# Optimization experiments

Measured on AMD Instinct MI355X. Metric: run time of the kernel, lower is better.

Reference implementation:

```python
import jax, jax.numpy as jnp
import numpy as np

N_NODES = 100000
N_EDGES = 600000
D = 128


def setup_inputs() -> dict:
    key = jax.random.key(0)
    k1, k2, k3, k4, k5, k6 = jax.random.split(key, 6)
    feat = jax.random.normal(k1, (N_NODES, D), dtype=jnp.float32)
    src = jax.random.randint(k2, (N_EDGES,), 0, N_NODES, dtype=jnp.int64)
    dst = jax.random.randint(k3, (N_EDGES,), 0, N_NODES, dtype=jnp.int64)
    W_neigh = jax.random.normal(k4, (D, D), dtype=jnp.float32) * (1.0 / np.sqrt(D))
    b_neigh = jax.random.normal(k5, (D,), dtype=jnp.float32) * 0.02
    W_self = jax.random.normal(k6, (D, D), dtype=jnp.float32) * (1.0 / np.sqrt(D))
    return {"feat": feat, "src": src, "dst": dst,
            "W_neigh": W_neigh, "b_neigh": b_neigh, "W_self": W_self}


def reference(feat, src, dst, W_neigh, b_neigh, W_self):
    # DGL GraphConv(norm='none'): sum-aggregate neighbor features, then linear.
    # agg[i] = sum_{(s->i) in E} feat[s]
    agg = jax.ops.segment_sum(feat[src], dst, num_segments=feat.shape[0])  # [N, D]
    neigh_feat = agg @ W_neigh + b_neigh                                   # [N, Dout]
    self_feat = feat @ W_self                                              # [N, Dout]
    return neigh_feat + self_feat
```

## Files before the change

kernel.cpp:

```cpp
#include <hip/hip_runtime.h>

#define DF 128
#define CAP 16
#define GR 64

typedef __attribute__((ext_vector_type(8))) short short8;
typedef __attribute__((ext_vector_type(4))) float v4f;

__device__ __forceinline__ unsigned short f2bf(float x) {
    unsigned u = __float_as_uint(x);
    unsigned r = (u + 0x7FFFu + ((u >> 16) & 1u)) >> 16;
    return (unsigned short)r;
}
__device__ __forceinline__ float bf2f(unsigned short h) {
    return __uint_as_float((unsigned)h << 16);
}
__device__ __forceinline__ unsigned pack2(float a, float b) {
    return (unsigned)f2bf(a) | ((unsigned)f2bf(b) << 16);
}

__global__ __launch_bounds__(256) void prep_kernel(
    const int* __restrict__ idx32, int nE, int* __restrict__ hdr,
    const float* __restrict__ Wn, const float* __restrict__ Ws,
    unsigned short* __restrict__ Bt, int* __restrict__ counts, int cnt_ints)
{
    const int b = blockIdx.x;
    const int t = threadIdx.x;
    if (b == 0) {
        __shared__ int sh;
        if (t == 0) sh = 0;
        __syncthreads();
        int found = 0;
        for (int i = t; i < 2048 && i < nE; i += 256)
            if (idx32[2 * i + 1] != 0) found = 1;
        if (found) sh = 1;
        __syncthreads();
        if (t == 0) { hdr[0] = sh; hdr[1] = 0; }
    } else if (b <= 128) {
        int idx = (b - 1) * 256 + t;
        int n = idx >> 7, k = idx & 127;
        float v = (n < DF) ? Wn[(size_t)k * DF + n] : Ws[(size_t)k * DF + (n - DF)];
        Bt[idx] = f2bf(v);
    } else {
        int off = ((b - 129) * 256 + t) * 4;
        if (off < cnt_ints)
            *reinterpret_cast<int4*>(counts + off) = make_int4(0, 0, 0, 0);
    }
}

__global__ __launch_bounds__(256) void fused_kernel(
    const float* __restrict__ feat, const unsigned short* __restrict__ Bt,
    const float* __restrict__ bias, unsigned short* __restrict__ Ybf,
    float* __restrict__ out, int M,
    const void* __restrict__ src, const void* __restrict__ dst, int nE,
    int* __restrict__ hdr, int* __restrict__ counts, int* __restrict__ buckets,
    int2* __restrict__ ovf)
{
    const int t   = threadIdx.x;
    const int bid = blockIdx.x;
    const int nb  = (int)gridDim.x;

    {
        const int e0 = (int)((long long)bid * nE / nb);
        const int e1 = (int)((long long)(bid + 1) * nE / nb);
        const int is32 = hdr[0];
        if (is32) {
            const int* sp = (const int*)src;
            const int* dp = (const int*)dst;
            for (int e = e0 + t; e < e1; e += 256) {
                int s = sp[e], d = dp[e];
                int pos = atomicAdd(&counts[d], 1);
                if (pos < CAP) {
                    buckets[(size_t)d * CAP + pos] = s;
                } else {
                    int oi = atomicAdd(&hdr[1], 1);
                    ovf[oi] = make_int2(s, d);
                }
            }
        } else {
            const long long* sp = (const long long*)src;
            const long long* dp = (const long long*)dst;
            for (int e = e0 + t; e < e1; e += 256) {
                int s = (int)sp[e], d = (int)dp[e];
                int pos = atomicAdd(&counts[d], 1);
                if (pos < CAP) {
                    buckets[(size_t)d * CAP + pos] = s;
                } else {
                    int oi = atomicAdd(&hdr[1], 1);
                    ovf[oi] = make_int2(s, d);
                }
            }
        }
    }

    __shared__ unsigned short As[GR][136];
    __shared__ unsigned short Ys[GR][136];

    const int wave = t >> 6;
    const int lane = t & 63;
    const int nl   = lane & 15;
    const int quad = lane >> 4;
    const int block_row = bid * GR;

    {
        const float* base = feat + (size_t)block_row * DF;
#pragma unroll
        for (int it = 0; it < 8; it++) {
            const int idx = t * 4 + it * 1024;
            const int row = idx >> 7, col = idx & 127;
            float4 v;
            if (block_row + row < M)
                v = *reinterpret_cast<const float4*>(base + idx);
            else
                v = make_float4(0.f, 0.f, 0.f, 0.f);
            uint2 pk;
            pk.x = pack2(v.x, v.y);
            pk.y = pack2(v.z, v.w);
            *reinterpret_cast<uint2*>(&As[row][col]) = pk;
        }
    }

    const int n0 = wave * 64;
    short8 bfrag[4][4];
#pragma unroll
    for (int ct = 0; ct < 4; ct++)
#pragma unroll
        for (int kk = 0; kk < 4; kk++)
            bfrag[ct][kk] = *reinterpret_cast<const short8*>(
                Bt + (size_t)(n0 + ct * 16 + nl) * DF + kk * 32 + quad * 8);

    float bcol[4];
#pragma unroll
    for (int ct = 0; ct < 4; ct++) {
        int n = n0 + ct * 16 + nl;
        bcol[ct] = (n >= DF) ? bias[n - DF] : 0.f;
    }

    __syncthreads();

#pragma unroll
    for (int rt = 0; rt < 4; rt++) {
        short8 afrag[4];
#pragma unroll
        for (int kk = 0; kk < 4; kk++)
            afrag[kk] = *reinterpret_cast<const short8*>(
                &As[rt * 16 + nl][kk * 32 + quad * 8]);
#pragma unroll
        for (int ct = 0; ct < 4; ct++) {
            v4f acc = {0.f, 0.f, 0.f, 0.f};
#pragma unroll
            for (int kk = 0; kk < 4; kk++)
                acc = __builtin_amdgcn_mfma_f32_16x16x32_bf16(
                    afrag[kk], bfrag[ct][kk], acc, 0, 0, 0);
            const int n = n0 + ct * 16 + nl;
            const int lrow = rt * 16 + quad * 4;
            if (n < DF) {
#pragma unroll
                for (int r = 0; r < 4; r++)
                    Ys[lrow + r][n] = f2bf(acc[r]);
            } else {
#pragma unroll
                for (int r = 0; r < 4; r++) {
                    const int grow = block_row + lrow + r;
                    if (grow < M)
                        out[(size_t)grow * DF + (n - DF)] = acc[r] + bcol[ct];
                }
            }
        }
    }

    __syncthreads();

    {
        const int row = t >> 2;
        const int cb  = (t & 3) * 32;
        const int grow = block_row + row;
        if (grow < M) {
            const uint4* srcp = reinterpret_cast<const uint4*>(&Ys[row][cb]);
            uint4* dstp = reinterpret_cast<uint4*>(Ybf + (size_t)grow * DF + cb);
            dstp[0] = srcp[0];
            dstp[1] = srcp[1];
            dstp[2] = srcp[2];
            dstp[3] = srcp[3];
        }
    }
}

__global__ __launch_bounds__(256) void gather_kernel(
    const unsigned short* __restrict__ Ybf,
    const int* __restrict__ counts, const int* __restrict__ buckets,
    const int* __restrict__ hdr, const int2* __restrict__ ovf,
    float* __restrict__ out, int M, int ngroups)
{
    const int gid  = blockIdx.x * 256 + threadIdx.x;
    const int grp  = gid >> 4;
    const int lane = gid & 15;
    const size_t lo = (size_t)lane * 8;

#define LDY(s) (*reinterpret_cast<const uint4*>(Ybf + (size_t)(s) * DF + lo))
#define ACC8(Y) do { \
        a0 += bf2f((unsigned short)((Y).x)); a1 += bf2f((unsigned short)((Y).x >> 16)); \
        a2 += bf2f((unsigned short)((Y).y)); a3 += bf2f((unsigned short)((Y).y >> 16)); \
        a4 += bf2f((unsigned short)((Y).z)); a5 += bf2f((unsigned short)((Y).z >> 16)); \
        a6 += bf2f((unsigned short)((Y).w)); a7 += bf2f((unsigned short)((Y).w >> 16)); \
    } while (0)

    if (grp < M) {
        const int node = grp;
        const int deg_raw = counts[node];
        const int deg = min(deg_raw, CAP);
        const int* b = buckets + (size_t)node * CAP;

        float a0 = 0.f, a1 = 0.f, a2 = 0.f, a3 = 0.f;
        float a4 = 0.f, a5 = 0.f, a6 = 0.f, a7 = 0.f;

        int4 sa = *reinterpret_cast<const int4*>(b);
        int4 sb = *reinterpret_cast<const int4*>(b + 4);
        uint4 y0, y1, y2, y3, y4, y5, y6, y7;
        if (0 < deg) y0 = LDY(sa.x);
        if (1 < deg) y1 = LDY(sa.y);
        if (2 < deg) y2 = LDY(sa.z);
        if (3 < deg) y3 = LDY(sa.w);
        if (4 < deg) y4 = LDY(sb.x);
        if (5 < deg) y5 = LDY(sb.y);
        if (6 < deg) y6 = LDY(sb.z);
        if (7 < deg) y7 = LDY(sb.w);
        if (0 < deg) ACC8(y0);
        if (1 < deg) ACC8(y1);
        if (2 < deg) ACC8(y2);
        if (3 < deg) ACC8(y3);
        if (4 < deg) ACC8(y4);
        if (5 < deg) ACC8(y5);
        if (6 < deg) ACC8(y6);
        if (7 < deg) ACC8(y7);

        if (deg > 8) {
            int4 sc = *reinterpret_cast<const int4*>(b + 8);
            int4 sd = *reinterpret_cast<const int4*>(b + 12);
            uint4 z0, z1, z2, z3, z4, z5, z6, z7;
            if ( 8 < deg) z0 = LDY(sc.x);
            if ( 9 < deg) z1 = LDY(sc.y);
            if (10 < deg) z2 = LDY(sc.z);
            if (11 < deg) z3 = LDY(sc.w);
            if (12 < deg) z4 = LDY(sd.x);
            if (13 < deg) z5 = LDY(sd.y);
            if (14 < deg) z6 = LDY(sd.z);
            if (15 < deg) z7 = LDY(sd.w);
            if ( 8 < deg) ACC8(z0);
            if ( 9 < deg) ACC8(z1);
            if (10 < deg) ACC8(z2);
            if (11 < deg) ACC8(z3);
            if (12 < deg) ACC8(z4);
            if (13 < deg) ACC8(z5);
            if (14 < deg) ACC8(z6);
            if (15 < deg) ACC8(z7);
        }

        float* op = out + (size_t)node * DF + lo;
        if (deg_raw <= CAP) {
            float4 o0 = *reinterpret_cast<const float4*>(op);
            float4 o1 = *reinterpret_cast<const float4*>(op + 4);
            o0.x += a0; o0.y += a1; o0.z += a2; o0.w += a3;
            o1.x += a4; o1.y += a5; o1.z += a6; o1.w += a7;
            *reinterpret_cast<float4*>(op)     = o0;
            *reinterpret_cast<float4*>(op + 4) = o1;
        } else {
            unsafeAtomicAdd(op + 0, a0);
            unsafeAtomicAdd(op + 1, a1);
            unsafeAtomicAdd(op + 2, a2);
            unsafeAtomicAdd(op + 3, a3);
            unsafeAtomicAdd(op + 4, a4);
            unsafeAtomicAdd(op + 5, a5);
            unsafeAtomicAdd(op + 6, a6);
            unsafeAtomicAdd(op + 7, a7);
        }
    }

    int n_ovf = hdr[1];
    for (int i = grp; i < n_ovf; i += ngroups) {
        int2 sd = ovf[i];
        uint4 y = LDY(sd.x);
        float* p = out + (size_t)sd.y * DF + lo;
        unsafeAtomicAdd(p + 0, bf2f((unsigned short)(y.x)));
        unsafeAtomicAdd(p + 1, bf2f((unsigned short)(y.x >> 16)));
        unsafeAtomicAdd(p + 2, bf2f((unsigned short)(y.y)));
        unsafeAtomicAdd(p + 3, bf2f((unsigned short)(y.y >> 16)));
        unsafeAtomicAdd(p + 4, bf2f((unsigned short)(y.z)));
        unsafeAtomicAdd(p + 5, bf2f((unsigned short)(y.z >> 16)));
        unsafeAtomicAdd(p + 6, bf2f((unsigned short)(y.w)));
        unsafeAtomicAdd(p + 7, bf2f((unsigned short)(y.w >> 16)));
    }
#undef LDY
#undef ACC8
}

extern "C" void kernel_launch(void* const* d_in, const int* in_sizes, int n_in,
                              void* d_out, int out_size, void* d_ws, size_t ws_size,
                              hipStream_t stream) {
    const float* feat = (const float*)d_in[0];
    const void*  src  = d_in[1];
    const void*  dst  = d_in[2];
    const float* Wn   = (const float*)d_in[3];
    const float* bias = (const float*)d_in[4];
    const float* Wsf  = (const float*)d_in[5];
    float* out = (float*)d_out;

    const int M  = in_sizes[0] / DF;
    const int nE = in_sizes[1];

    const size_t cnt_off   = 256;
    const size_t cnt_bytes = (((size_t)(M + 1) * 4) + 255) & ~(size_t)255;
    const size_t bkt_off   = cnt_off + cnt_bytes;
    const size_t bkt_bytes = (size_t)M * CAP * sizeof(int);
    const size_t bt_off    = (bkt_off + bkt_bytes + 255) & ~(size_t)255;
    const size_t bt_bytes  = (size_t)256 * DF * sizeof(unsigned short);
    const size_t y_off     = bt_off + bt_bytes;
    const size_t y_bytes   = (size_t)M * DF * sizeof(unsigned short);
    const size_t ovf_off   = (y_off + y_bytes + 255) & ~(size_t)255;

    int*            hdr     = (int*)d_ws;
    int*            counts  = (int*)((char*)d_ws + cnt_off);
    int*            buckets = (int*)((char*)d_ws + bkt_off);
    unsigned short* Bt      = (unsigned short*)((char*)d_ws + bt_off);
    unsigned short* Ybf     = (unsigned short*)((char*)d_ws + y_off);
    int2*           ovf     = (int2*)((char*)d_ws + ovf_off);

    const int cnt_ints = (int)(cnt_bytes / 4);
    const int nzb = (cnt_ints + 1023) / 1024;
    prep_kernel<<<1 + 128 + nzb, 256, 0, stream>>>(
        (const int*)src, nE, hdr, Wn, Wsf, Bt, counts, cnt_ints);

    const int gemm_blocks = (M + GR - 1) / GR;
    fused_kernel<<<gemm_blocks, 256, 0, stream>>>(
        feat, Bt, bias, Ybf, out, M, src, dst, nE,
        hdr, counts, buckets, ovf);

    const int gablocks = (int)(((long long)M * 16 + 255) / 256);
    const int ngroups  = gablocks * 16;
    gather_kernel<<<gablocks, 256, 0, stream>>>(
        Ybf, counts, buckets, hdr, ovf, out, M, ngroups);
}
```

Before: 204.5 us.

## Merge scatter, GEMM and gather into a persistent cooperative kernel

Replaces the fused scatter+GEMM launch and the separate gather launch with one persistent cooperative kernel. Blocks pull work items (edge-placement slices and GEMM tiles) from an atomic counter, then meet at a grid-wide sync before a grid-stride gather. The gather now loads the out rows early and adds scheduling barriers to group its loads ahead of the accumulation. This saves a kernel launch and its tail, at the cost of grid-sync overhead and occupancy limits (launch_bounds 256,4). A fallback two-kernel path runs if the cooperative launch fails.

Result: slower. 348.3 us (+70.3%).

```diff
diff --git a/kernel.cpp b/kernel.cpp
--- a/kernel.cpp
+++ b/kernel.cpp
@@ -1,8 +1,12 @@
 #include <hip/hip_runtime.h>
+#include <hip/hip_cooperative_groups.h>
+
+namespace cg = cooperative_groups;
 
 #define DF 128
 #define CAP 16
 #define GR 64
+#define PSLICES 256
 
 typedef __attribute__((ext_vector_type(8))) short short8;
 typedef __attribute__((ext_vector_type(4))) float v4f;
@@ -35,7 +39,7 @@
             if (idx32[2 * i + 1] != 0) found = 1;
         if (found) sh = 1;
         __syncthreads();
-        if (t == 0) { hdr[0] = sh; hdr[1] = 0; }
+        if (t == 0) { hdr[0] = sh; hdr[1] = 0; hdr[2] = 0; }
     } else if (b <= 128) {
         int idx = (b - 1) * 256 + t;
         int n = idx >> 7, k = idx & 127;
@@ -48,59 +52,54 @@
     }
 }
 
-__global__ __launch_bounds__(256) void fused_kernel(
-    const float* __restrict__ feat, const unsigned short* __restrict__ Bt,
-    const float* __restrict__ bias, unsigned short* __restrict__ Ybf,
-    float* __restrict__ out, int M,
-    const void* __restrict__ src, const void* __restrict__ dst, int nE,
-    int* __restrict__ hdr, int* __restrict__ counts, int* __restrict__ buckets,
-    int2* __restrict__ ovf)
-{
-    const int t   = threadIdx.x;
-    const int bid = blockIdx.x;
-    const int nb  = (int)gridDim.x;
-
-    {
-        const int e0 = (int)((long long)bid * nE / nb);
-        const int e1 = (int)((long long)(bid + 1) * nE / nb);
-        const int is32 = hdr[0];
-        if (is32) {
-            const int* sp = (const int*)src;
-            const int* dp = (const int*)dst;
-            for (int e = e0 + t; e < e1; e += 256) {
-                int s = sp[e], d = dp[e];
-                int pos = atomicAdd(&counts[d], 1);
-                if (pos < CAP) {
-                    buckets[(size_t)d * CAP + pos] = s;
-                } else {
-                    int oi = atomicAdd(&hdr[1], 1);
-                    ovf[oi] = make_int2(s, d);
-                }
+__device__ __forceinline__ void place_slice(
+    int T, int t, const void* __restrict__ src, const void* __restrict__ dst,
+    int nE, int* __restrict__ hdr, int* __restrict__ counts,
+    int* __restrict__ buckets, int2* __restrict__ ovf)
+{
+    const int e0 = (int)((long long)T * nE / PSLICES);
+    const int e1 = (int)((long long)(T + 1) * nE / PSLICES);
+    const int is32 = hdr[0];
+    if (is32) {
+        const int* sp = (const int*)src;
+        const int* dp = (const int*)dst;
+        for (int e = e0 + t; e < e1; e += 256) {
+            int s = sp[e], d = dp[e];
+            int pos = atomicAdd(&counts[d], 1);
+            if (pos < CAP) {
+                buckets[(size_t)d * CAP + pos] = s;
+            } else {
+                int oi = atomicAdd(&hdr[1], 1);
+                ovf[oi] = make_int2(s, d);
             }
-        } else {
-            const long long* sp = (const long long*)src;
-            const long long* dp = (const long long*)dst;
-            for (int e = e0 + t; e < e1; e += 256) {
-                int s = (int)sp[e], d = (int)dp[e];
-                int pos = atomicAdd(&counts[d], 1);
-                if (pos < CAP) {
-                    buckets[(size_t)d * CAP + pos] = s;
-                } else {
-                    int oi = atomicAdd(&hdr[1], 1);
-                    ovf[oi] = make_int2(s, d);
-                }
+        }
+    } else {
+        const long long* sp = (const long long*)src;
+        const long long* dp = (const long long*)dst;
+        for (int e = e0 + t; e < e1; e += 256) {
+            int s = (int)sp[e], d = (int)dp[e];
+            int pos = atomicAdd(&counts[d], 1);
+            if (pos < CAP) {
+                buckets[(size_t)d * CAP + pos] = s;
+            } else {
+                int oi = atomicAdd(&hdr[1], 1);
+                ovf[oi] = make_int2(s, d);
             }
         }
     }
-
-    __shared__ unsigned short As[GR][136];
-    __shared__ unsigned short Ys[GR][136];
-
+}
+
+__device__ __forceinline__ void gemm_tile(
+    int tile, int t, const float* __restrict__ feat,
+    const unsigned short* __restrict__ Bt, const float* __restrict__ bias,
+    unsigned short* __restrict__ Ybf, float* __restrict__ out, int M,
+    unsigned short (*As)[136], unsigned short (*Ys)[136])
+{
     const int wave = t >> 6;
     const int lane = t & 63;
     const int nl   = lane & 15;
     const int quad = lane >> 4;
-    const int block_row = bid * GR;
+    const int block_row = tile * GR;
 
     {
         const float* base = feat + (size_t)block_row * DF;
@@ -186,17 +185,6 @@
     }
 }
 
-__global__ __launch_bounds__(256) void gather_kernel(
-    const unsigned short* __restrict__ Ybf,
-    const int* __restrict__ counts, const int* __restrict__ buckets,
-    const int* __restrict__ hdr, const int2* __restrict__ ovf,
-    float* __restrict__ out, int M, int ngroups)
-{
-    const int gid  = blockIdx.x * 256 + threadIdx.x;
-    const int grp  = gid >> 4;
-    const int lane = gid & 15;
-    const size_t lo = (size_t)lane * 8;
-
 #define LDY(s) (*reinterpret_cast<const uint4*>(Ybf + (size_t)(s) * DF + lo))
 #define ACC8(Y) do { \
         a0 += bf2f((unsigned short)((Y).x)); a1 += bf2f((unsigned short)((Y).x >> 16)); \
@@ -205,17 +193,32 @@
         a6 += bf2f((unsigned short)((Y).w)); a7 += bf2f((unsigned short)((Y).w >> 16)); \
     } while (0)
 
-    if (grp < M) {
+__device__ __forceinline__ void gather_all(
+    int bid, int nblocks, int t,
+    const unsigned short* __restrict__ Ybf, const int* __restrict__ counts,
+    const int* __restrict__ buckets, const int* __restrict__ hdr,
+    const int2* __restrict__ ovf, float* __restrict__ out, int M)
+{
+    const int lane = t & 15;
+    const size_t lo = (size_t)lane * 8;
+    const int chunks = (M * 16 + 255) / 256;
+
+    for (int c = bid; c < chunks; c += nblocks) {
+        const int grp = c * 16 + (t >> 4);
+        if (grp >= M) continue;
         const int node = grp;
         const int deg_raw = counts[node];
         const int deg = min(deg_raw, CAP);
         const int* b = buckets + (size_t)node * CAP;
+        float* op = out + (size_t)node * DF + lo;
 
         float a0 = 0.f, a1 = 0.f, a2 = 0.f, a3 = 0.f;
         float a4 = 0.f, a5 = 0.f, a6 = 0.f, a7 = 0.f;
 
         int4 sa = *reinterpret_cast<const int4*>(b);
         int4 sb = *reinterpret_cast<const int4*>(b + 4);
+        float4 o0 = *reinterpret_cast<const float4*>(op);
+        float4 o1 = *reinterpret_cast<const float4*>(op + 4);
         uint4 y0, y1, y2, y3, y4, y5, y6, y7;
         if (0 < deg) y0 = LDY(sa.x);
         if (1 < deg) y1 = LDY(sa.y);
@@ -225,6 +228,7 @@
         if (5 < deg) y5 = LDY(sb.y);
         if (6 < deg) y6 = LDY(sb.z);
         if (7 < deg) y7 = LDY(sb.w);
+        __builtin_amdgcn_sched_barrier(0);
         if (0 < deg) ACC8(y0);
         if (1 < deg) ACC8(y1);
         if (2 < deg) ACC8(y2);
@@ -246,6 +250,7 @@
             if (13 < deg) z5 = LDY(sd.y);
             if (14 < deg) z6 = LDY(sd.z);
             if (15 < deg) z7 = LDY(sd.w);
+            __builtin_amdgcn_sched_barrier(0);
             if ( 8 < deg) ACC8(z0);
             if ( 9 < deg) ACC8(z1);
             if (10 < deg) ACC8(z2);
@@ -256,10 +261,7 @@
             if (15 < deg) ACC8(z7);
         }
 
-        float* op = out + (size_t)node * DF + lo;
         if (deg_raw <= CAP) {
-            float4 o0 = *reinterpret_cast<const float4*>(op);
-            float4 o1 = *reinterpret_cast<const float4*>(op + 4);
             o0.x += a0; o0.y += a1; o0.z += a2; o0.w += a3;
             o1.x += a4; o1.y += a5; o1.z += a6; o1.w += a7;
             *reinterpret_cast<float4*>(op)     = o0;
@@ -276,8 +278,9 @@
         }
     }
 
-    int n_ovf = hdr[1];
-    for (int i = grp; i < n_ovf; i += ngroups) {
+    const int n_ovf = hdr[1];
+    const int gstride = nblocks * 16;
+    for (int i = bid * 16 + (t >> 4); i < n_ovf; i += gstride) {
         int2 sd = ovf[i];
         uint4 y = LDY(sd.x);
         float* p = out + (size_t)sd.y * DF + lo;
@@ -290,8 +293,66 @@
         unsafeAtomicAdd(p + 6, bf2f((unsigned short)(y.w)));
         unsafeAtomicAdd(p + 7, bf2f((unsigned short)(y.w >> 16)));
     }
+}
 #undef LDY
 #undef ACC8
+
+__global__ __launch_bounds__(256, 4) void coop_kernel(
+    const float* __restrict__ feat, const unsigned short* __restrict__ Bt,
+    const float* __restrict__ bias, unsigned short* __restrict__ Ybf,
+    float* __restrict__ out, int M,
+    const void* __restrict__ src, const void* __restrict__ dst, int nE,
+    int* __restrict__ hdr, int* __restrict__ counts, int* __restrict__ buckets,
+    int2* __restrict__ ovf, int ntiles)
+{
+    __shared__ unsigned short As[GR][136];
+    __shared__ unsigned short Ys[GR][136];
+    __shared__ int sh_t;
+    const int t = threadIdx.x;
+    const int NT = PSLICES + ntiles;
+
+    for (;;) {
+        __syncthreads();
+        if (t == 0) sh_t = atomicAdd(&hdr[2], 1);
+        __syncthreads();
+        const int T = sh_t;
+        if (T >= NT) break;
+        if (T < PSLICES)
+            place_slice(T, t, src, dst, nE, hdr, counts, buckets, ovf);
+        else
+            gemm_tile(T - PSLICES, t, feat, Bt, bias, Ybf, out, M, As, Ys);
+    }
+
+    cg::this_grid().sync();
+
+    gather_all((int)blockIdx.x, (int)gridDim.x, t,
+               Ybf, counts, buckets, hdr, ovf, out, M);
+}
+
+__global__ __launch_bounds__(256) void fb_fused_kernel(
+    const float* __restrict__ feat, const unsigned short* __restrict__ Bt,
+    const float* __restrict__ bias, unsigned short* __restrict__ Ybf,
+    float* __restrict__ out, int M,
+    const void* __restrict__ src, const void* __restrict__ dst, int nE,
+    int* __restrict__ hdr, int* __restrict__ counts, int* __restrict__ buckets,
+    int2* __restrict__ ovf)
+{
+    __shared__ unsigned short As[GR][136];
+    __shared__ unsigned short Ys[GR][136];
+    const int t = threadIdx.x;
+    if (blockIdx.x < PSLICES)
+        place_slice(blockIdx.x, t, src, dst, nE, hdr, counts, buckets, ovf);
+    else
+        gemm_tile(blockIdx.x - PSLICES, t, feat, Bt, bias, Ybf, out, M, As, Ys);
+}
+
+__global__ __launch_bounds__(256) void fb_gather_kernel(
+    const unsigned short* __restrict__ Ybf, const int* __restrict__ counts,
+    const int* __restrict__ buckets, const int* __restrict__ hdr,
+    const int2* __restrict__ ovf, float* __restrict__ out, int M)
+{
+    gather_all((int)blockIdx.x, (int)gridDim.x, (int)threadIdx.x,
+               Ybf, counts, buckets, hdr, ovf, out, M);
 }
 
 extern "C" void kernel_launch(void* const* d_in, const int* in_sizes, int n_in,
@@ -305,8 +366,8 @@
     const float* Wsf  = (const float*)d_in[5];
     float* out = (float*)d_out;
 
-    const int M  = in_sizes[0] / DF;
-    const int nE = in_sizes[1];
+    int M  = in_sizes[0] / DF;
+    int nE = in_sizes[1];
 
     const size_t cnt_off   = 256;
     const size_t cnt_bytes = (((size_t)(M + 1) * 4) + 255) & ~(size_t)255;
@@ -330,13 +391,46 @@
     prep_kernel<<<1 + 128 + nzb, 256, 0, stream>>>(
         (const int*)src, nE, hdr, Wn, Wsf, Bt, counts, cnt_ints);
 
-    const int gemm_blocks = (M + GR - 1) / GR;
-    fused_kernel<<<gemm_blocks, 256, 0, stream>>>(
-        feat, Bt, bias, Ybf, out, M, src, dst, nE,
-        hdr, counts, buckets, ovf);
-
-    const int gablocks = (int)(((long long)M * 16 + 255) / 256);
-    const int ngroups  = gablocks * 16;
-    gather_kernel<<<gablocks, 256, 0, stream>>>(
-        Ybf, counts, buckets, hdr, ovf, out, M, ngroups);
-}
+    int ntiles = (M + GR - 1) / GR;
+
+    static int s_mode = 0;
+    static int s_nblocks = 1024;
+    if (s_mode == 0) {
+        int occ = 0;
+        hipError_t e1 = hipOccupancyMaxActiveBlocksPerMultiprocessor(
+            &occ, coop_kernel, 256, 0);
+        int ncu = 256;
+        hipDeviceProp_t prop;
+        int dev = 0;
+        if (hipGetDevice(&dev) == hipSuccess &&
+            hipGetDeviceProperties(&prop, dev) == hipSuccess)
+            ncu = prop.multiProcessorCount;
+        if (e1 == hipSuccess && occ > 0) {
+            s_nblocks = occ * ncu;
+            s_mode = 1;
+        } else {
+            s_mode = -1;
+        }
+    }
+
+    if (s_mode == 1) {
+        void* args[] = {
+            (void*)&feat, (void*)&Bt, (void*)&bias, (void*)&Ybf, (void*)&out,
+            (void*)&M, (void*)&src, (void*)&dst, (void*)&nE,
+            (void*)&hdr, (void*)&counts, (void*)&buckets, (void*)&ovf,
+            (void*)&ntiles };
+        hipError_t e = hipLaunchCooperativeKernel(
+            (const void*)coop_kernel, dim3(s_nblocks), dim3(256),
+            args, 0, stream);
+        if (e != hipSuccess) s_mode = -1;
+    }
+
+    if (s_mode == -1) {
+        fb_fused_kernel<<<PSLICES + ntiles, 256, 0, stream>>>(
+            feat, Bt, bias, Ybf, out, M, src, dst, nE,
+            hdr, counts, buckets, ovf);
+        const int gablocks = (int)(((long long)M * 16 + 255) / 256);
+        fb_gather_kernel<<<gablocks, 256, 0, stream>>>(
+            Ybf, counts, buckets, hdr, ovf, out, M);
+    }
+}
```

## Split edge bucketing into dedicated blocks and make gather loads branch-free

Applied to the files above, without the earlier changes.

The edge-bucketing work moves out of every GEMM block into 256 dedicated grid-strided blocks that return early, so GEMM blocks no longer serialize atomic bucketing before their matmul. In the gather kernel, unused neighbor slots are redirected to a zeroed padding row at index M. All eight row loads and the output read are then issued unconditionally before a sched_barrier, which removes divergent branches and increases memory-level parallelism. The cost is extra loads of the zero row for low-degree nodes, plus one extra Ybf row zeroed in the prep kernel.

Result: faster. 193.9 us (-5.2%).

```diff
diff --git a/kernel.cpp b/kernel.cpp
--- a/kernel.cpp
+++ b/kernel.cpp
@@ -3,6 +3,7 @@
 #define DF 128
 #define CAP 16
 #define GR 64
+#define PBLK 256
 
 typedef __attribute__((ext_vector_type(8))) short short8;
 typedef __attribute__((ext_vector_type(4))) float v4f;
@@ -22,7 +23,8 @@
 __global__ __launch_bounds__(256) void prep_kernel(
     const int* __restrict__ idx32, int nE, int* __restrict__ hdr,
     const float* __restrict__ Wn, const float* __restrict__ Ws,
-    unsigned short* __restrict__ Bt, int* __restrict__ counts, int cnt_ints)
+    unsigned short* __restrict__ Bt, int* __restrict__ counts, int cnt_ints,
+    unsigned short* __restrict__ Ybf, int M)
 {
     const int b = blockIdx.x;
     const int t = threadIdx.x;
@@ -36,6 +38,8 @@
         if (found) sh = 1;
         __syncthreads();
         if (t == 0) { hdr[0] = sh; hdr[1] = 0; }
+        if (t < 64)
+            reinterpret_cast<unsigned*>(Ybf + (size_t)M * DF)[t] = 0u;
     } else if (b <= 128) {
         int idx = (b - 1) * 256 + t;
         int n = idx >> 7, k = idx & 127;
@@ -56,18 +60,15 @@
     int* __restrict__ hdr, int* __restrict__ counts, int* __restrict__ buckets,
     int2* __restrict__ ovf)
 {
-    const int t   = threadIdx.x;
-    const int bid = blockIdx.x;
-    const int nb  = (int)gridDim.x;
-
-    {
-        const int e0 = (int)((long long)bid * nE / nb);
-        const int e1 = (int)((long long)(bid + 1) * nE / nb);
+    const int t = threadIdx.x;
+
+    if (blockIdx.x < PBLK) {
         const int is32 = hdr[0];
+        const int stride = PBLK * 256;
         if (is32) {
             const int* sp = (const int*)src;
             const int* dp = (const int*)dst;
-            for (int e = e0 + t; e < e1; e += 256) {
+            for (int e = blockIdx.x * 256 + t; e < nE; e += stride) {
                 int s = sp[e], d = dp[e];
                 int pos = atomicAdd(&counts[d], 1);
                 if (pos < CAP) {
@@ -80,7 +81,7 @@
         } else {
             const long long* sp = (const long long*)src;
             const long long* dp = (const long long*)dst;
-            for (int e = e0 + t; e < e1; e += 256) {
+            for (int e = blockIdx.x * 256 + t; e < nE; e += stride) {
                 int s = (int)sp[e], d = (int)dp[e];
                 int pos = atomicAdd(&counts[d], 1);
                 if (pos < CAP) {
@@ -91,6 +92,7 @@
                 }
             }
         }
+        return;
     }
 
     __shared__ unsigned short As[GR][136];
@@ -100,7 +102,7 @@
     const int lane = t & 63;
     const int nl   = lane & 15;
     const int quad = lane >> 4;
-    const int block_row = bid * GR;
+    const int block_row = (blockIdx.x - PBLK) * GR;
 
     {
         const float* base = feat + (size_t)block_row * DF;
@@ -210,56 +212,61 @@
         const int deg_raw = counts[node];
         const int deg = min(deg_raw, CAP);
         const int* b = buckets + (size_t)node * CAP;
+        float* op = out + (size_t)node * DF + lo;
 
         float a0 = 0.f, a1 = 0.f, a2 = 0.f, a3 = 0.f;
         float a4 = 0.f, a5 = 0.f, a6 = 0.f, a7 = 0.f;
 
         int4 sa = *reinterpret_cast<const int4*>(b);
         int4 sb = *reinterpret_cast<const int4*>(b + 4);
-        uint4 y0, y1, y2, y3, y4, y5, y6, y7;
-        if (0 < deg) y0 = LDY(sa.x);
-        if (1 < deg) y1 = LDY(sa.y);
-        if (2 < deg) y2 = LDY(sa.z);
-        if (3 < deg) y3 = LDY(sa.w);
-        if (4 < deg) y4 = LDY(sb.x);
-        if (5 < deg) y5 = LDY(sb.y);
-        if (6 < deg) y6 = LDY(sb.z);
-        if (7 < deg) y7 = LDY(sb.w);
-        if (0 < deg) ACC8(y0);
-        if (1 < deg) ACC8(y1);
-        if (2 < deg) ACC8(y2);
-        if (3 < deg) ACC8(y3);
-        if (4 < deg) ACC8(y4);
-        if (5 < deg) ACC8(y5);
-        if (6 < deg) ACC8(y6);
-        if (7 < deg) ACC8(y7);
+        const int i0 = (0 < deg) ? sa.x : M;
+        const int i1 = (1 < deg) ? sa.y : M;
+        const int i2 = (2 < deg) ? sa.z : M;
+        const int i3 = (3 < deg) ? sa.w : M;
+        const int i4 = (4 < deg) ? sb.x : M;
+        const int i5 = (5 < deg) ? sb.y : M;
+        const int i6 = (6 < deg) ? sb.z : M;
+        const int i7 = (7 < deg) ? sb.w : M;
+
+        uint4 y0 = LDY(i0);
+        uint4 y1 = LDY(i1);
+        uint4 y2 = LDY(i2);
+        uint4 y3 = LDY(i3);
+        uint4 y4 = LDY(i4);
+        uint4 y5 = LDY(i5);
+        uint4 y6 = LDY(i6);
+        uint4 y7 = LDY(i7);
+        float4 o0 = *reinterpret_cast<const float4*>(op);
+        float4 o1 = *reinterpret_cast<const float4*>(op + 4);
+        __builtin_amdgcn_sched_barrier(0);
+        ACC8(y0); ACC8(y1); ACC8(y2); ACC8(y3);
+        ACC8(y4); ACC8(y5); ACC8(y6); ACC8(y7);
 
         if (deg > 8) {
             int4 sc = *reinterpret_cast<const int4*>(b + 8);
             int4 sd = *reinterpret_cast<const int4*>(b + 12);
-            uint4 z0, z1, z2, z3, z4, z5, z6, z7;
-            if ( 8 < deg) z0 = LDY(sc.x);
-            if ( 9 < deg) z1 = LDY(sc.y);
-            if (10 < deg) z2 = LDY(sc.z);
-            if (11 < deg) z3 = LDY(sc.w);
-            if (12 < deg) z4 = LDY(sd.x);
-            if (13 < deg) z5 = LDY(sd.y);
-            if (14 < deg) z6 = LDY(sd.z);
-            if (15 < deg) z7 = LDY(sd.w);
-            if ( 8 < deg) ACC8(z0);
-            if ( 9 < deg) ACC8(z1);
-            if (10 < deg) ACC8(z2);
-            if (11 < deg) ACC8(z3);
-            if (12 < deg) ACC8(z4);
-            if (13 < deg) ACC8(z5);
-            if (14 < deg) ACC8(z6);
-            if (15 < deg) ACC8(z7);
-        }
-
-        float* op = out + (size_t)node * DF + lo;
+            const int j0 = ( 8 < deg) ? sc.x : M;
+            const int j1 = ( 9 < deg) ? sc.y : M;
+            const int j2 = (10 < deg) ? sc.z : M;
+            const int j3 = (11 < deg) ? sc.w : M;
+            const int j4 = (12 < deg) ? sd.x : M;
+            const int j5 = (13 < deg) ? sd.y : M;
+            const int j6 = (14 < deg) ? sd.z : M;
+            const int j7 = (15 < deg) ? sd.w : M;
+            uint4 z0 = LDY(j0);
+            uint4 z1 = LDY(j1);
+            uint4 z2 = LDY(j2);
+            uint4 z3 = LDY(j3);
+            uint4 z4 = LDY(j4);
+            uint4 z5 = LDY(j5);
+            uint4 z6 = LDY(j6);
+            uint4 z7 = LDY(j7);
+            __builtin_amdgcn_sched_barrier(0);
+            ACC8(z0); ACC8(z1); ACC8(z2); ACC8(z3);
+            ACC8(z4); ACC8(z5); ACC8(z6); ACC8(z7);
+        }
+
         if (deg_raw <= CAP) {
-            float4 o0 = *reinterpret_cast<const float4*>(op);
-            float4 o1 = *reinterpret_cast<const float4*>(op + 4);
             o0.x += a0; o0.y += a1; o0.z += a2; o0.w += a3;
             o1.x += a4; o1.y += a5; o1.z += a6; o1.w += a7;
             *reinterpret_cast<float4*>(op)     = o0;
@@ -315,7 +322,7 @@
     const size_t bt_off    = (bkt_off + bkt_bytes + 255) & ~(size_t)255;
     const size_t bt_bytes  = (size_t)256 * DF * sizeof(unsigned short);
     const size_t y_off     = bt_off + bt_bytes;
-    const size_t y_bytes   = (size_t)M * DF * sizeof(unsigned short);
+    const size_t y_bytes   = (size_t)(M + 1) * DF * sizeof(unsigned short);
     const size_t ovf_off   = (y_off + y_bytes + 255) & ~(size_t)255;
 
     int*            hdr     = (int*)d_ws;
@@ -328,15 +335,15 @@
     const int cnt_ints = (int)(cnt_bytes / 4);
     const int nzb = (cnt_ints + 1023) / 1024;
     prep_kernel<<<1 + 128 + nzb, 256, 0, stream>>>(
-        (const int*)src, nE, hdr, Wn, Wsf, Bt, counts, cnt_ints);
+        (const int*)src, nE, hdr, Wn, Wsf, Bt, counts, cnt_ints, Ybf, M);
 
     const int gemm_blocks = (M + GR - 1) / GR;
-    fused_kernel<<<gemm_blocks, 256, 0, stream>>>(
+    fused_kernel<<<PBLK + gemm_blocks, 256, 0, stream>>>(
         feat, Bt, bias, Ybf, out, M, src, dst, nE,
         hdr, counts, buckets, ovf);
 
     const int gablocks = (int)(((long long)M * 16 + 255) / 256);
-    const int ngroups  = gablocks * 16;
+    const int ngroups = gablocks * 16;
     gather_kernel<<<gablocks, 256, 0, stream>>>(
         Ybf, counts, buckets, hdr, ovf, out, M, ngroups);
 }
```
